# Performance work log

Hardware: AMD Instinct MI355X
Metric: run time of the kernel (lower is better)

Reference implementation:

```python
import jax, jax.numpy as jnp
import numpy as np

# Segment geometry (from init_kwargs): modes ['u','uv','v'] -> out_v = alpha * x_u @ W_uv
U = 128
V = 128
IN_OFF = [0, 128, 256, 384]
W_OFF = [k * U * V for k in range(8)]          # [0,16384,...,114688]
OUT_OFF = [0, 128, 256, 384]
IN_STRIDE = 512
OUT_STRIDE = 512
W_STRIDE = 8 * U * V                           # 131072
# (in_seg, w_seg, out_seg, coefficient)
PATHS = [(0, 0, 0, 1.0), (1, 1, 1, 1.0), (2, 2, 2, 1.0), (3, 3, 3, 1.0),
         (0, 4, 1, 0.5), (1, 5, 2, 0.5), (2, 6, 3, 0.5), (3, 7, 0, 0.5)]
B = 32768
E = 4  # num_embeddings (experts)


def setup_inputs() -> dict:
    key = jax.random.key(0)
    k1, k2, k3 = jax.random.split(key, 3)
    tensor_in = jax.random.normal(k1, (B, IN_STRIDE), dtype=jnp.float32)
    tensor_w = jax.random.normal(k2, (E, W_STRIDE), dtype=jnp.float32)
    tensor_w_id = jax.random.randint(k3, (B,), 0, E, dtype=jnp.int32)
    return {"tensor_in": tensor_in, "tensor_w": tensor_w, "tensor_w_id": tensor_w_id}


def _batch_linear(tensor_in, tensor_w, tensor_w_id):
    """Segmented path-indexed grouped linear (cuEquivariance BatchLinear fwd).

    tensor_in: [B, IN_STRIDE]; tensor_w: [E, W_STRIDE]; tensor_w_id: [B] int in [0,E).
    For each path (i, j, k, alpha):
        out[b, OUT_OFF[k]:+V] += alpha * x[b, IN_OFF[i]:+U] @ W[w_id[b], seg j].reshape(U, V)
    """
    nb = tensor_in.shape[0]
    ne = tensor_w.shape[0]
    onehot = jax.nn.one_hot(tensor_w_id, ne, dtype=tensor_in.dtype)  # [B, E]
    out = jnp.zeros((nb, OUT_STRIDE), dtype=tensor_in.dtype)
    for (i, j, k, a) in PATHS:
        x = tensor_in[:, IN_OFF[i]:IN_OFF[i] + U]                    # [B, U]
        w_seg = tensor_w[:, W_OFF[j]:W_OFF[j] + U * V].reshape(ne, U, V)
        # masked per-expert dense GEMMs (small fixed expert count)
        y = jnp.zeros((nb, V), dtype=tensor_in.dtype)
        for e in range(ne):
            y = y + onehot[:, e:e + 1] * (x @ w_seg[e])              # [B, V]
        out = out.at[:, OUT_OFF[k]:OUT_OFF[k] + V].add(a * y)
    return out


def reference(tensor_in, tensor_w, tensor_w_id):
    return _batch_linear(tensor_in, tensor_w, tensor_w_id)
```

## Files before the change

kernel.cpp:

```cpp
#include <hip/hip_runtime.h>
#include <stdint.h>

#define U 128
#define V 128
#define IN_STRIDE 512
#define OUT_STRIDE 512
#define W_STRIDE (8 * U * V)
#define NB 32768
#define NE 4

#define WS_WSHUF 0
#define WS_CNT   1048576
#define WS_SORT  1048640

typedef __bf16 bf16x8 __attribute__((ext_vector_type(8)));
typedef float f32x16 __attribute__((ext_vector_type(16)));
typedef unsigned int u32x4 __attribute__((ext_vector_type(4)));

static __device__ __forceinline__ unsigned short f2bf(float f) {
    unsigned int u = __builtin_bit_cast(unsigned int, f);
    u += 0x7FFFu + ((u >> 16) & 1u);
    return (unsigned short)(u >> 16);
}

__global__ void prep_kernel(const float* __restrict__ w, unsigned short* __restrict__ wshuf,
                            unsigned int* __restrict__ cnt) {
    if (blockIdx.x == 0 && threadIdx.x < NE) cnt[threadIdx.x] = 0u;
    int t = blockIdx.x * 256 + threadIdx.x;
    int lane = t & 63;
    int kt = (t >> 6) & 7;
    int nt = (t >> 9) & 3;
    int s  = (t >> 11) & 7;
    int e  = (t >> 14) & 3;
    int kbase = kt * 16 + ((lane >> 5) << 3);
    int n = nt * 32 + (lane & 31);
    const float* src = w + (size_t)e * W_STRIDE + (size_t)s * (U * V) + n;
    float sc = (s >= 4) ? 0.5f : 1.0f;
    __attribute__((aligned(16))) unsigned short o[8];
#pragma unroll
    for (int j = 0; j < 8; j++) o[j] = f2bf(src[(size_t)(kbase + j) * V] * sc);
    *(u32x4*)(wshuf + (size_t)t * 8) = *(const u32x4*)o;
}

__global__ void scatter_kernel(const int* __restrict__ wid, unsigned int* __restrict__ cnt,
                               int* __restrict__ sorted) {
    __shared__ unsigned int lcnt[NE];
    __shared__ unsigned int lbase[NE];
    int t = threadIdx.x;
    if (t < NE) lcnt[t] = 0u;
    __syncthreads();
    int i = blockIdx.x * 256 + t;
    int e = wid[i];
    unsigned int lpos = atomicAdd(&lcnt[e], 1u);
    __syncthreads();
    if (t < NE) lbase[t] = atomicAdd(&cnt[t], lcnt[t]);
    __syncthreads();
    sorted[e * NB + (int)(lbase[e] + lpos)] = i;
}

__global__ __launch_bounds__(512, 4) void gemm_kernel(
        const float* __restrict__ x, const unsigned short* __restrict__ wshuf,
        const unsigned int* __restrict__ cnt, const int* __restrict__ sorted,
        float* __restrict__ out) {
    const int rowbase = blockIdx.x * 32;
    __shared__ float ldsf[32][512];
    __shared__ int rowid[32];

    const unsigned int p1 = cnt[0];
    const unsigned int p2 = p1 + cnt[1];
    const unsigned int p3 = p2 + cnt[2];

    const int t = threadIdx.x;
    const int w = t >> 6, lane = t & 63;
    const int l5 = lane >> 5, m0 = lane & 31;
    const int kout = w >> 1, nhalf = w & 1;

    int rid[4];
#pragma unroll
    for (int i = 0; i < 4; i++) {
        unsigned int ls = (unsigned int)(rowbase + 4 * w + i);
        int e = (ls >= p1) + (ls >= p2) + (ls >= p3);
        unsigned int pe = (e == 0) ? 0u : (e == 1) ? p1 : (e == 2) ? p2 : p3;
        rid[i] = sorted[e * NB + (int)(ls - pe)];
    }
    if (t < 32) {
        unsigned int ls = (unsigned int)(rowbase + t);
        int e = (ls >= p1) + (ls >= p2) + (ls >= p3);
        unsigned int pe = (e == 0) ? 0u : (e == 1) ? p1 : (e == 2) ? p2 : p3;
        rowid[t] = sorted[e * NB + (int)(ls - pe)];
    }

#pragma unroll
    for (int i = 0; i < 4; i++) {
        int r = 4 * w + i;
        int rs = r & 7;
        const float* xb = x + (size_t)rid[i] * IN_STRIDE + ((m0 ^ rs) << 2) + l5 * 128;
#pragma unroll
        for (int h = 0; h < 2; h++) {
            __builtin_amdgcn_global_load_lds(
                (const __attribute__((address_space(1))) unsigned int*)(xb + h * 256),
                (__attribute__((address_space(3))) unsigned int*)&ldsf[r][h * 256],
                16, 0, 0);
        }
    }

    const unsigned int lh = (unsigned int)rowbase, lt = (unsigned int)(rowbase + 31);
    const int ehead = (lh >= p1) + (lh >= p2) + (lh >= p3);
    const int etail = (lt >= p1) + (lt >= p2) + (lt >= p3);
    const unsigned int l0 = (unsigned int)(rowbase + m0);
    const int e0 = (l0 >= p1) + (l0 >= p2) + (l0 >= p3);

    const int xbc1 = (kout + 3) & 3;
    const int xbs[2] = {kout, xbc1};
    const int sgs[2] = {kout, xbc1 + 4};
    const int rsw = m0 & 7;

    f32x16 acc0 = {}, acc1 = {};

    if (ehead == etail) {
        const unsigned short* wb0 =
            wshuf + (size_t)(((ehead * 8 + sgs[0]) * 4 + nhalf * 2) * 8) * 512 + (size_t)lane * 8;
        u32x4 bp[8];
#pragma unroll
        for (int kt = 0; kt < 4; kt++) {
            bp[kt * 2]     = *(const u32x4*)(wb0 + (size_t)kt * 512);
            bp[kt * 2 + 1] = *(const u32x4*)(wb0 + (size_t)(8 + kt) * 512);
        }
        __syncthreads();

#pragma unroll
        for (int c = 0; c < 2; c++) {
            const float* ar = &ldsf[m0][xbs[c] * 128];
            const unsigned short* wb =
                wshuf + (size_t)(((ehead * 8 + sgs[c]) * 4 + nhalf * 2) * 8) * 512 + (size_t)lane * 8;
#pragma unroll
            for (int kt = 0; kt < 8; kt++) {
                int gj0 = kt * 4 + l5 * 2;
                float4 va = *(const float4*)(ar + ((gj0 ^ rsw) << 2));
                float4 vb = *(const float4*)(ar + (((gj0 + 1) ^ rsw) << 2));
                bf16x8 a;
                a[0] = (__bf16)va.x; a[1] = (__bf16)va.y;
                a[2] = (__bf16)va.z; a[3] = (__bf16)va.w;
                a[4] = (__bf16)vb.x; a[5] = (__bf16)vb.y;
                a[6] = (__bf16)vb.z; a[7] = (__bf16)vb.w;
                bf16x8 b0, b1;
                if (c == 0 && kt < 4) {
                    b0 = __builtin_bit_cast(bf16x8, bp[kt * 2]);
                    b1 = __builtin_bit_cast(bf16x8, bp[kt * 2 + 1]);
                } else {
                    b0 = __builtin_bit_cast(bf16x8, *(const u32x4*)(wb + (size_t)kt * 512));
                    b1 = __builtin_bit_cast(bf16x8, *(const u32x4*)(wb + (size_t)(8 + kt) * 512));
                }
                acc0 = __builtin_amdgcn_mfma_f32_32x32x16_bf16(a, b0, acc0, 0, 0, 0);
                acc1 = __builtin_amdgcn_mfma_f32_32x32x16_bf16(a, b1, acc1, 0, 0, 0);
            }
        }
    } else {
        unsigned int msk[4];
#pragma unroll
        for (int e = 0; e < 4; e++) msk[e] = (e0 == e) ? 0xFFFFFFFFu : 0u;
        __syncthreads();
#pragma unroll
        for (int c = 0; c < 2; c++) {
            const float* ar = &ldsf[m0][xbs[c] * 128];
#pragma unroll
            for (int kt = 0; kt < 8; kt++) {
                int gj0 = kt * 4 + l5 * 2;
                float4 va = *(const float4*)(ar + ((gj0 ^ rsw) << 2));
                float4 vb = *(const float4*)(ar + (((gj0 + 1) ^ rsw) << 2));
                __attribute__((aligned(16))) unsigned short au[8];
                au[0] = f2bf(va.x); au[1] = f2bf(va.y);
                au[2] = f2bf(va.z); au[3] = f2bf(va.w);
                au[4] = f2bf(vb.x); au[5] = f2bf(vb.y);
                au[6] = f2bf(vb.z); au[7] = f2bf(vb.w);
                u32x4 araw = *(const u32x4*)au;
#pragma unroll
                for (int e = 0; e < 4; e++) {
                    u32x4 mm = {msk[e], msk[e], msk[e], msk[e]};
                    bf16x8 am = __builtin_bit_cast(bf16x8, araw & mm);
                    const unsigned short* wb =
                        wshuf + (size_t)(((e * 8 + sgs[c]) * 4 + nhalf * 2) * 8) * 512 + (size_t)lane * 8;
                    bf16x8 b0 = __builtin_bit_cast(bf16x8, *(const u32x4*)(wb + (size_t)kt * 512));
                    bf16x8 b1 = __builtin_bit_cast(bf16x8, *(const u32x4*)(wb + (size_t)(8 + kt) * 512));
                    acc0 = __builtin_amdgcn_mfma_f32_32x32x16_bf16(am, b0, acc0, 0, 0, 0);
                    acc1 = __builtin_amdgcn_mfma_f32_32x32x16_bf16(am, b1, acc1, 0, 0, 0);
                }
            }
        }
    }

    const int colb = kout * 128 + nhalf * 64 + m0;
    const int rh = l5 << 2;
#pragma unroll
    for (int q = 0; q < 4; q++) {
#pragma unroll
        for (int d = 0; d < 4; d++) {
            int reg = q * 4 + d;
            int rl = d + 8 * q + rh;
            float* o = out + (size_t)rowid[rl] * OUT_STRIDE + colb;
            o[0]  = acc0[reg];
            o[32] = acc1[reg];
        }
    }
}

extern "C" void kernel_launch(void* const* d_in, const int* in_sizes, int n_in,
                              void* d_out, int out_size, void* d_ws, size_t ws_size,
                              hipStream_t stream) {
    const float* x = (const float*)d_in[0];
    const float* w = (const float*)d_in[1];
    const int* wid = (const int*)d_in[2];
    float* out = (float*)d_out;

    unsigned short* wshuf = (unsigned short*)((char*)d_ws + WS_WSHUF);
    unsigned int* cnt = (unsigned int*)((char*)d_ws + WS_CNT);
    int* sorted = (int*)((char*)d_ws + WS_SORT);

    prep_kernel<<<256, 256, 0, stream>>>(w, wshuf, cnt);
    scatter_kernel<<<128, 256, 0, stream>>>(wid, cnt, sorted);
    gemm_kernel<<<1024, 512, 0, stream>>>(x, wshuf, cnt, sorted, out);
}
```

Baseline: 136.7 us.

## Switch GEMM to 16-row tiles with 16x16x32 MFMA and reshuffled weight layout

Halves the rows per block from 32 to 16 and switches from 32x32x16 to 16x16x32 bf16 MFMA, which changes the prep kernel's weight-shuffle layout to match the new B-fragment shape. The grid doubles to 2048 blocks with half the LDS per block, and launch bounds rise to 8 blocks per CU. The aim is higher occupancy and fewer blocks straddling expert boundaries, which take the slow masked four-expert path. The cost is that each weight fragment is reused over only 16 rows, roughly doubling weight reads per output row.

```diff
diff --git a/kernel.cpp b/kernel.cpp
--- a/kernel.cpp
+++ b/kernel.cpp
@@ -14,7 +14,7 @@
 #define WS_SORT  1048640
 
 typedef __bf16 bf16x8 __attribute__((ext_vector_type(8)));
-typedef float f32x16 __attribute__((ext_vector_type(16)));
+typedef float f32x4 __attribute__((ext_vector_type(4)));
 typedef unsigned int u32x4 __attribute__((ext_vector_type(4)));
 
 static __device__ __forceinline__ unsigned short f2bf(float f) {
@@ -28,12 +28,12 @@
     if (blockIdx.x == 0 && threadIdx.x < NE) cnt[threadIdx.x] = 0u;
     int t = blockIdx.x * 256 + threadIdx.x;
     int lane = t & 63;
-    int kt = (t >> 6) & 7;
-    int nt = (t >> 9) & 3;
+    int ks = (t >> 6) & 3;
+    int nt = (t >> 8) & 7;
     int s  = (t >> 11) & 7;
     int e  = (t >> 14) & 3;
-    int kbase = kt * 16 + ((lane >> 5) << 3);
-    int n = nt * 32 + (lane & 31);
+    int kbase = ks * 32 + ((lane >> 4) << 3);
+    int n = nt * 16 + (lane & 15);
     const float* src = w + (size_t)e * W_STRIDE + (size_t)s * (U * V) + n;
     float sc = (s >= 4) ? 0.5f : 1.0f;
     __attribute__((aligned(16))) unsigned short o[8];
@@ -58,13 +58,13 @@
     sorted[e * NB + (int)(lbase[e] + lpos)] = i;
 }
 
-__global__ __launch_bounds__(512, 4) void gemm_kernel(
+__global__ __launch_bounds__(512, 8) void gemm_kernel(
         const float* __restrict__ x, const unsigned short* __restrict__ wshuf,
         const unsigned int* __restrict__ cnt, const int* __restrict__ sorted,
         float* __restrict__ out) {
-    const int rowbase = blockIdx.x * 32;
-    __shared__ float ldsf[32][512];
-    __shared__ int rowid[32];
+    const int rowbase = blockIdx.x * 16;
+    __shared__ float ldsf[16][512];
+    __shared__ int rowid[16];
 
     const unsigned int p1 = cnt[0];
     const unsigned int p2 = p1 + cnt[1];
@@ -74,16 +74,18 @@
     const int w = t >> 6, lane = t & 63;
     const int l5 = lane >> 5, m0 = lane & 31;
     const int kout = w >> 1, nhalf = w & 1;
-
-    int rid[4];
-#pragma unroll
-    for (int i = 0; i < 4; i++) {
-        unsigned int ls = (unsigned int)(rowbase + 4 * w + i);
+    const int m16 = lane & 15;
+    const int kg = lane >> 4;
+
+    int rid[2];
+#pragma unroll
+    for (int i = 0; i < 2; i++) {
+        unsigned int ls = (unsigned int)(rowbase + 2 * w + i);
         int e = (ls >= p1) + (ls >= p2) + (ls >= p3);
         unsigned int pe = (e == 0) ? 0u : (e == 1) ? p1 : (e == 2) ? p2 : p3;
         rid[i] = sorted[e * NB + (int)(ls - pe)];
     }
-    if (t < 32) {
+    if (t < 16) {
         unsigned int ls = (unsigned int)(rowbase + t);
         int e = (ls >= p1) + (ls >= p2) + (ls >= p3);
         unsigned int pe = (e == 0) ? 0u : (e == 1) ? p1 : (e == 2) ? p2 : p3;
@@ -91,10 +93,10 @@
     }
 
 #pragma unroll
-    for (int i = 0; i < 4; i++) {
-        int r = 4 * w + i;
+    for (int i = 0; i < 2; i++) {
+        int r = 2 * w + i;
         int rs = r & 7;
-        const float* xb = x + (size_t)rid[i] * IN_STRIDE + ((m0 ^ rs) << 2) + l5 * 128;
+        const float* xb = x + (size_t)rid[i] * IN_STRIDE + l5 * 128 + ((m0 ^ rs) << 2);
 #pragma unroll
         for (int h = 0; h < 2; h++) {
             __builtin_amdgcn_global_load_lds(
@@ -104,38 +106,39 @@
         }
     }
 
-    const unsigned int lh = (unsigned int)rowbase, lt = (unsigned int)(rowbase + 31);
+    const unsigned int lh = (unsigned int)rowbase, lt = (unsigned int)(rowbase + 15);
     const int ehead = (lh >= p1) + (lh >= p2) + (lh >= p3);
     const int etail = (lt >= p1) + (lt >= p2) + (lt >= p3);
-    const unsigned int l0 = (unsigned int)(rowbase + m0);
+    const unsigned int l0 = (unsigned int)(rowbase + m16);
     const int e0 = (l0 >= p1) + (l0 >= p2) + (l0 >= p3);
 
     const int xbc1 = (kout + 3) & 3;
     const int xbs[2] = {kout, xbc1};
     const int sgs[2] = {kout, xbc1 + 4};
-    const int rsw = m0 & 7;
-
-    f32x16 acc0 = {}, acc1 = {};
+    const int rsw = m16 & 7;
+
+    f32x4 acc[4] = {};
 
     if (ehead == etail) {
         const unsigned short* wb0 =
-            wshuf + (size_t)(((ehead * 8 + sgs[0]) * 4 + nhalf * 2) * 8) * 512 + (size_t)lane * 8;
-        u32x4 bp[8];
-#pragma unroll
-        for (int kt = 0; kt < 4; kt++) {
-            bp[kt * 2]     = *(const u32x4*)(wb0 + (size_t)kt * 512);
-            bp[kt * 2 + 1] = *(const u32x4*)(wb0 + (size_t)(8 + kt) * 512);
-        }
+            wshuf + ((size_t)((ehead * 8 + sgs[0]) * 8 + nhalf * 4)) * 2048 + (size_t)lane * 8;
+        const unsigned short* wb1 =
+            wshuf + ((size_t)((ehead * 8 + sgs[1]) * 8 + nhalf * 4)) * 2048 + (size_t)lane * 8;
+        u32x4 bp[4];
+#pragma unroll
+        for (int ni = 0; ni < 4; ni++)
+            bp[ni] = *(const u32x4*)(wb0 + (size_t)ni * 2048);
+
         __syncthreads();
 
 #pragma unroll
         for (int c = 0; c < 2; c++) {
-            const float* ar = &ldsf[m0][xbs[c] * 128];
-            const unsigned short* wb =
-                wshuf + (size_t)(((ehead * 8 + sgs[c]) * 4 + nhalf * 2) * 8) * 512 + (size_t)lane * 8;
-#pragma unroll
-            for (int kt = 0; kt < 8; kt++) {
-                int gj0 = kt * 4 + l5 * 2;
+            const float* ar = &ldsf[m16][0];
+            const int cb3 = xbs[c] * 32;
+            const unsigned short* wb = (c == 0) ? wb0 : wb1;
+#pragma unroll
+            for (int s = 0; s < 4; s++) {
+                int gj0 = cb3 + s * 8 + kg * 2;
                 float4 va = *(const float4*)(ar + ((gj0 ^ rsw) << 2));
                 float4 vb = *(const float4*)(ar + (((gj0 + 1) ^ rsw) << 2));
                 bf16x8 a;
@@ -143,16 +146,14 @@
                 a[2] = (__bf16)va.z; a[3] = (__bf16)va.w;
                 a[4] = (__bf16)vb.x; a[5] = (__bf16)vb.y;
                 a[6] = (__bf16)vb.z; a[7] = (__bf16)vb.w;
-                bf16x8 b0, b1;
-                if (c == 0 && kt < 4) {
-                    b0 = __builtin_bit_cast(bf16x8, bp[kt * 2]);
-                    b1 = __builtin_bit_cast(bf16x8, bp[kt * 2 + 1]);
-                } else {
-                    b0 = __builtin_bit_cast(bf16x8, *(const u32x4*)(wb + (size_t)kt * 512));
-                    b1 = __builtin_bit_cast(bf16x8, *(const u32x4*)(wb + (size_t)(8 + kt) * 512));
+#pragma unroll
+                for (int ni = 0; ni < 4; ni++) {
+                    bf16x8 b;
+                    if (c == 0 && s == 0) b = __builtin_bit_cast(bf16x8, bp[ni]);
+                    else b = __builtin_bit_cast(bf16x8,
+                             *(const u32x4*)(wb + (size_t)ni * 2048 + (size_t)s * 512));
+                    acc[ni] = __builtin_amdgcn_mfma_f32_16x16x32_bf16(a, b, acc[ni], 0, 0, 0);
                 }
-                acc0 = __builtin_amdgcn_mfma_f32_32x32x16_bf16(a, b0, acc0, 0, 0, 0);
-                acc1 = __builtin_amdgcn_mfma_f32_32x32x16_bf16(a, b1, acc1, 0, 0, 0);
             }
         }
     } else {
@@ -162,10 +163,11 @@
         __syncthreads();
 #pragma unroll
         for (int c = 0; c < 2; c++) {
-            const float* ar = &ldsf[m0][xbs[c] * 128];
-#pragma unroll
-            for (int kt = 0; kt < 8; kt++) {
-                int gj0 = kt * 4 + l5 * 2;
+            const float* ar = &ldsf[m16][0];
+            const int cb3 = xbs[c] * 32;
+#pragma unroll
+            for (int s = 0; s < 4; s++) {
+                int gj0 = cb3 + s * 8 + kg * 2;
                 float4 va = *(const float4*)(ar + ((gj0 ^ rsw) << 2));
                 float4 vb = *(const float4*)(ar + (((gj0 + 1) ^ rsw) << 2));
                 __attribute__((aligned(16))) unsigned short au[8];
@@ -178,28 +180,26 @@
                 for (int e = 0; e < 4; e++) {
                     u32x4 mm = {msk[e], msk[e], msk[e], msk[e]};
                     bf16x8 am = __builtin_bit_cast(bf16x8, araw & mm);
-                    const unsigned short* wb =
-                        wshuf + (size_t)(((e * 8 + sgs[c]) * 4 + nhalf * 2) * 8) * 512 + (size_t)lane * 8;
-                    bf16x8 b0 = __builtin_bit_cast(bf16x8, *(const u32x4*)(wb + (size_t)kt * 512));
-                    bf16x8 b1 = __builtin_bit_cast(bf16x8, *(const u32x4*)(wb + (size_t)(8 + kt) * 512));
-                    acc0 = __builtin_amdgcn_mfma_f32_32x32x16_bf16(am, b0, acc0, 0, 0, 0);
-                    acc1 = __builtin_amdgcn_mfma_f32_32x32x16_bf16(am, b1, acc1, 0, 0, 0);
+                    const unsigned short* wbe =
+                        wshuf + ((size_t)((e * 8 + sgs[c]) * 8 + nhalf * 4)) * 2048 + (size_t)lane * 8;
+#pragma unroll
+                    for (int ni = 0; ni < 4; ni++) {
+                        bf16x8 b = __builtin_bit_cast(bf16x8,
+                            *(const u32x4*)(wbe + (size_t)ni * 2048 + (size_t)s * 512));
+                        acc[ni] = __builtin_amdgcn_mfma_f32_16x16x32_bf16(am, b, acc[ni], 0, 0, 0);
+                    }
                 }
             }
         }
     }
 
-    const int colb = kout * 128 + nhalf * 64 + m0;
-    const int rh = l5 << 2;
-#pragma unroll
-    for (int q = 0; q < 4; q++) {
-#pragma unroll
-        for (int d = 0; d < 4; d++) {
-            int reg = q * 4 + d;
-            int rl = d + 8 * q + rh;
-            float* o = out + (size_t)rowid[rl] * OUT_STRIDE + colb;
-            o[0]  = acc0[reg];
-            o[32] = acc1[reg];
+    const int colb = w * 64 + m16;
+#pragma unroll
+    for (int ni = 0; ni < 4; ni++) {
+#pragma unroll
+        for (int reg = 0; reg < 4; reg++) {
+            int rl = kg * 4 + reg;
+            out[(size_t)rowid[rl] * OUT_STRIDE + colb + ni * 16] = acc[ni][reg];
         }
     }
 }
@@ -218,5 +218,5 @@
 
     prep_kernel<<<256, 256, 0, stream>>>(w, wshuf, cnt);
     scatter_kernel<<<128, 256, 0, stream>>>(wid, cnt, sorted);
-    gemm_kernel<<<1024, 512, 0, stream>>>(x, wshuf, cnt, sorted, out);
-}
+    gemm_kernel<<<2048, 512, 0, stream>>>(x, wshuf, cnt, sorted, out);
+}
```

Result: slower. 165.6 us (+21.2%).

## Process four row tiles per block with double-buffered LDS prefetch of activations

Applied to the files above, without the earlier changes.

Each GEMM block now handles 128 sorted rows as four 32-row tiles, using two LDS buffers so the gathered x rows for the next tile are loaded while the current tile computes. Output stores for the previous tile are deferred into the next iteration, and the full first weight segment is preloaded into registers. The grid shrinks fourfold and launch bounds drop to two blocks per CU, trading cross-block parallelism and occupancy for intra-block load/compute overlap and amortised setup.

```diff
diff --git a/kernel.cpp b/kernel.cpp
--- a/kernel.cpp
+++ b/kernel.cpp
@@ -58,13 +58,13 @@
     sorted[e * NB + (int)(lbase[e] + lpos)] = i;
 }
 
-__global__ __launch_bounds__(512, 4) void gemm_kernel(
+__global__ __launch_bounds__(512, 2) void gemm_kernel(
         const float* __restrict__ x, const unsigned short* __restrict__ wshuf,
         const unsigned int* __restrict__ cnt, const int* __restrict__ sorted,
         float* __restrict__ out) {
-    const int rowbase = blockIdx.x * 32;
-    __shared__ float ldsf[32][512];
-    __shared__ int rowid[32];
+    const int blk = blockIdx.x;
+    __shared__ float ldsf[2][32][512];
+    __shared__ int rowid[128];
 
     const unsigned int p1 = cnt[0];
     const unsigned int p2 = p1 + cnt[1];
@@ -74,17 +74,10 @@
     const int w = t >> 6, lane = t & 63;
     const int l5 = lane >> 5, m0 = lane & 31;
     const int kout = w >> 1, nhalf = w & 1;
-
-    int rid[4];
-#pragma unroll
-    for (int i = 0; i < 4; i++) {
-        unsigned int ls = (unsigned int)(rowbase + 4 * w + i);
-        int e = (ls >= p1) + (ls >= p2) + (ls >= p3);
-        unsigned int pe = (e == 0) ? 0u : (e == 1) ? p1 : (e == 2) ? p2 : p3;
-        rid[i] = sorted[e * NB + (int)(ls - pe)];
-    }
-    if (t < 32) {
-        unsigned int ls = (unsigned int)(rowbase + t);
+    const int rsw = m0 & 7;
+
+    if (t < 128) {
+        unsigned int ls = (unsigned int)(blk * 128 + t);
         int e = (ls >= p1) + (ls >= p2) + (ls >= p3);
         unsigned int pe = (e == 0) ? 0u : (e == 1) ? p1 : (e == 2) ? p2 : p3;
         rowid[t] = sorted[e * NB + (int)(ls - pe)];
@@ -93,115 +86,204 @@
 #pragma unroll
     for (int i = 0; i < 4; i++) {
         int r = 4 * w + i;
+        unsigned int ls = (unsigned int)(blk * 128 + r);
+        int e = (ls >= p1) + (ls >= p2) + (ls >= p3);
+        unsigned int pe = (e == 0) ? 0u : (e == 1) ? p1 : (e == 2) ? p2 : p3;
+        int rr = sorted[e * NB + (int)(ls - pe)];
         int rs = r & 7;
-        const float* xb = x + (size_t)rid[i] * IN_STRIDE + ((m0 ^ rs) << 2) + l5 * 128;
+        const float* xb = x + (size_t)rr * IN_STRIDE + ((m0 ^ rs) << 2) + l5 * 128;
 #pragma unroll
         for (int h = 0; h < 2; h++) {
             __builtin_amdgcn_global_load_lds(
                 (const __attribute__((address_space(1))) unsigned int*)(xb + h * 256),
-                (__attribute__((address_space(3))) unsigned int*)&ldsf[r][h * 256],
+                (__attribute__((address_space(3))) unsigned int*)&ldsf[0][r][h * 256],
                 16, 0, 0);
         }
     }
 
-    const unsigned int lh = (unsigned int)rowbase, lt = (unsigned int)(rowbase + 31);
-    const int ehead = (lh >= p1) + (lh >= p2) + (lh >= p3);
-    const int etail = (lt >= p1) + (lt >= p2) + (lt >= p3);
-    const unsigned int l0 = (unsigned int)(rowbase + m0);
-    const int e0 = (l0 >= p1) + (l0 >= p2) + (l0 >= p3);
-
-    const int xbc1 = (kout + 3) & 3;
-    const int xbs[2] = {kout, xbc1};
-    const int sgs[2] = {kout, xbc1 + 4};
-    const int rsw = m0 & 7;
-
+    asm volatile("s_waitcnt vmcnt(0) lgkmcnt(0)" ::: "memory");
+    __builtin_amdgcn_sched_barrier(0);
+    __builtin_amdgcn_s_barrier();
+    __builtin_amdgcn_sched_barrier(0);
+
+    const int colb = kout * 128 + nhalf * 64 + m0;
+    const int rh = l5 << 2;
     f32x16 acc0 = {}, acc1 = {};
 
-    if (ehead == etail) {
-        const unsigned short* wb0 =
-            wshuf + (size_t)(((ehead * 8 + sgs[0]) * 4 + nhalf * 2) * 8) * 512 + (size_t)lane * 8;
-        u32x4 bp[8];
-#pragma unroll
-        for (int kt = 0; kt < 4; kt++) {
-            bp[kt * 2]     = *(const u32x4*)(wb0 + (size_t)kt * 512);
-            bp[kt * 2 + 1] = *(const u32x4*)(wb0 + (size_t)(8 + kt) * 512);
+    for (int T = 0; T < 4; T++) {
+        const unsigned int rb = (unsigned int)(blk * 128 + T * 32);
+        const int ehead = (rb >= p1) + (rb >= p2) + (rb >= p3);
+        const unsigned int rte = rb + 31u;
+        const int etail = (rte >= p1) + (rte >= p2) + (rte >= p3);
+        const int fast = (ehead == etail);
+        const int xb1 = (kout + 3) & 3;
+        const float (*buf)[512] = ldsf[T & 1];
+
+        if (fast) {
+            const unsigned short* wb0 =
+                wshuf + (size_t)(((ehead * 8 + kout) * 4 + nhalf * 2) * 8) * 512 + (size_t)lane * 8;
+            u32x4 bp[16];
+#pragma unroll
+            for (int kt = 0; kt < 8; kt++) {
+                bp[kt * 2]     = *(const u32x4*)(wb0 + (size_t)kt * 512);
+                bp[kt * 2 + 1] = *(const u32x4*)(wb0 + (size_t)(8 + kt) * 512);
+            }
+
+            if (T > 0) {
+#pragma unroll
+                for (int q = 0; q < 4; q++)
+#pragma unroll
+                    for (int d = 0; d < 4; d++) {
+                        int reg = q * 4 + d;
+                        int rl = d + 8 * q + rh;
+                        float* o = out + (size_t)rowid[(T - 1) * 32 + rl] * OUT_STRIDE + colb;
+                        o[0]  = acc0[reg];
+                        o[32] = acc1[reg];
+                    }
+                acc0 = (f32x16){};
+                acc1 = (f32x16){};
+            }
+
+            if (T < 3) {
+#pragma unroll
+                for (int i = 0; i < 4; i++) {
+                    int r = 4 * w + i;
+                    int rr = rowid[(T + 1) * 32 + r];
+                    int rs = r & 7;
+                    const float* xb = x + (size_t)rr * IN_STRIDE + ((m0 ^ rs) << 2) + l5 * 128;
+#pragma unroll
+                    for (int h = 0; h < 2; h++) {
+                        __builtin_amdgcn_global_load_lds(
+                            (const __attribute__((address_space(1))) unsigned int*)(xb + h * 256),
+                            (__attribute__((address_space(3))) unsigned int*)&ldsf[(T + 1) & 1][r][h * 256],
+                            16, 0, 0);
+                    }
+                }
+            }
+
+            {
+                const float* ar = &buf[m0][kout * 128];
+#pragma unroll
+                for (int kt = 0; kt < 8; kt++) {
+                    int gj0 = kt * 4 + l5 * 2;
+                    float4 va = *(const float4*)(ar + ((gj0 ^ rsw) << 2));
+                    float4 vb = *(const float4*)(ar + (((gj0 + 1) ^ rsw) << 2));
+                    bf16x8 a;
+                    a[0] = (__bf16)va.x; a[1] = (__bf16)va.y;
+                    a[2] = (__bf16)va.z; a[3] = (__bf16)va.w;
+                    a[4] = (__bf16)vb.x; a[5] = (__bf16)vb.y;
+                    a[6] = (__bf16)vb.z; a[7] = (__bf16)vb.w;
+                    bf16x8 b0 = __builtin_bit_cast(bf16x8, bp[kt * 2]);
+                    bf16x8 b1 = __builtin_bit_cast(bf16x8, bp[kt * 2 + 1]);
+                    acc0 = __builtin_amdgcn_mfma_f32_32x32x16_bf16(a, b0, acc0, 0, 0, 0);
+                    acc1 = __builtin_amdgcn_mfma_f32_32x32x16_bf16(a, b1, acc1, 0, 0, 0);
+                }
+            }
+            {
+                const unsigned short* wb1 =
+                    wshuf + (size_t)(((ehead * 8 + xb1 + 4) * 4 + nhalf * 2) * 8) * 512 + (size_t)lane * 8;
+                const float* ar = &buf[m0][xb1 * 128];
+#pragma unroll
+                for (int kt = 0; kt < 8; kt++) {
+                    int gj0 = kt * 4 + l5 * 2;
+                    float4 va = *(const float4*)(ar + ((gj0 ^ rsw) << 2));
+                    float4 vb = *(const float4*)(ar + (((gj0 + 1) ^ rsw) << 2));
+                    bf16x8 a;
+                    a[0] = (__bf16)va.x; a[1] = (__bf16)va.y;
+                    a[2] = (__bf16)va.z; a[3] = (__bf16)va.w;
+                    a[4] = (__bf16)vb.x; a[5] = (__bf16)vb.y;
+                    a[6] = (__bf16)vb.z; a[7] = (__bf16)vb.w;
+                    bf16x8 b0 = __builtin_bit_cast(bf16x8, *(const u32x4*)(wb1 + (size_t)kt * 512));
+                    bf16x8 b1 = __builtin_bit_cast(bf16x8, *(const u32x4*)(wb1 + (size_t)(8 + kt) * 512));
+                    acc0 = __builtin_amdgcn_mfma_f32_32x32x16_bf16(a, b0, acc0, 0, 0, 0);
+                    acc1 = __builtin_amdgcn_mfma_f32_32x32x16_bf16(a, b1, acc1, 0, 0, 0);
+                }
+            }
+        } else {
+            if (T > 0) {
+#pragma unroll
+                for (int q = 0; q < 4; q++)
+#pragma unroll
+                    for (int d = 0; d < 4; d++) {
+                        int reg = q * 4 + d;
+                        int rl = d + 8 * q + rh;
+                        float* o = out + (size_t)rowid[(T - 1) * 32 + rl] * OUT_STRIDE + colb;
+                        o[0]  = acc0[reg];
+                        o[32] = acc1[reg];
+                    }
+                acc0 = (f32x16){};
+                acc1 = (f32x16){};
+            }
+            if (T < 3) {
+#pragma unroll
+                for (int i = 0; i < 4; i++) {
+                    int r = 4 * w + i;
+                    int rr = rowid[(T + 1) * 32 + r];
+                    int rs = r & 7;
+                    const float* xb = x + (size_t)rr * IN_STRIDE + ((m0 ^ rs) << 2) + l5 * 128;
+#pragma unroll
+                    for (int h = 0; h < 2; h++) {
+                        __builtin_amdgcn_global_load_lds(
+                            (const __attribute__((address_space(1))) unsigned int*)(xb + h * 256),
+                            (__attribute__((address_space(3))) unsigned int*)&ldsf[(T + 1) & 1][r][h * 256],
+                            16, 0, 0);
+                    }
+                }
+            }
+            const unsigned int l0 = rb + (unsigned int)m0;
+            const int e0 = (l0 >= p1) + (l0 >= p2) + (l0 >= p3);
+            unsigned int msk[4];
+#pragma unroll
+            for (int e = 0; e < 4; e++) msk[e] = (e0 == e) ? 0xFFFFFFFFu : 0u;
+            const int xbs[2] = {kout, xb1};
+            const int sgs[2] = {kout, xb1 + 4};
+#pragma unroll
+            for (int c = 0; c < 2; c++) {
+                const float* ar = &buf[m0][xbs[c] * 128];
+#pragma unroll
+                for (int kt = 0; kt < 8; kt++) {
+                    int gj0 = kt * 4 + l5 * 2;
+                    float4 va = *(const float4*)(ar + ((gj0 ^ rsw) << 2));
+                    float4 vb = *(const float4*)(ar + (((gj0 + 1) ^ rsw) << 2));
+                    __attribute__((aligned(16))) unsigned short au[8];
+                    au[0] = f2bf(va.x); au[1] = f2bf(va.y);
+                    au[2] = f2bf(va.z); au[3] = f2bf(va.w);
+                    au[4] = f2bf(vb.x); au[5] = f2bf(vb.y);
+                    au[6] = f2bf(vb.z); au[7] = f2bf(vb.w);
+                    u32x4 araw = *(const u32x4*)au;
+#pragma unroll
+                    for (int e = 0; e < 4; e++) {
+                        u32x4 mm = {msk[e], msk[e], msk[e], msk[e]};
+                        bf16x8 am = __builtin_bit_cast(bf16x8, araw & mm);
+                        const unsigned short* wbe =
+                            wshuf + (size_t)(((e * 8 + sgs[c]) * 4 + nhalf * 2) * 8) * 512 + (size_t)lane * 8;
+                        bf16x8 b0 = __builtin_bit_cast(bf16x8, *(const u32x4*)(wbe + (size_t)kt * 512));
+                        bf16x8 b1 = __builtin_bit_cast(bf16x8, *(const u32x4*)(wbe + (size_t)(8 + kt) * 512));
+                        acc0 = __builtin_amdgcn_mfma_f32_32x32x16_bf16(am, b0, acc0, 0, 0, 0);
+                        acc1 = __builtin_amdgcn_mfma_f32_32x32x16_bf16(am, b1, acc1, 0, 0, 0);
+                    }
+                }
+            }
         }
-        __syncthreads();
-
-#pragma unroll
-        for (int c = 0; c < 2; c++) {
-            const float* ar = &ldsf[m0][xbs[c] * 128];
-            const unsigned short* wb =
-                wshuf + (size_t)(((ehead * 8 + sgs[c]) * 4 + nhalf * 2) * 8) * 512 + (size_t)lane * 8;
-#pragma unroll
-            for (int kt = 0; kt < 8; kt++) {
-                int gj0 = kt * 4 + l5 * 2;
-                float4 va = *(const float4*)(ar + ((gj0 ^ rsw) << 2));
-                float4 vb = *(const float4*)(ar + (((gj0 + 1) ^ rsw) << 2));
-                bf16x8 a;
-                a[0] = (__bf16)va.x; a[1] = (__bf16)va.y;
-                a[2] = (__bf16)va.z; a[3] = (__bf16)va.w;
-                a[4] = (__bf16)vb.x; a[5] = (__bf16)vb.y;
-                a[6] = (__bf16)vb.z; a[7] = (__bf16)vb.w;
-                bf16x8 b0, b1;
-                if (c == 0 && kt < 4) {
-                    b0 = __builtin_bit_cast(bf16x8, bp[kt * 2]);
-                    b1 = __builtin_bit_cast(bf16x8, bp[kt * 2 + 1]);
-                } else {
-                    b0 = __builtin_bit_cast(bf16x8, *(const u32x4*)(wb + (size_t)kt * 512));
-                    b1 = __builtin_bit_cast(bf16x8, *(const u32x4*)(wb + (size_t)(8 + kt) * 512));
-                }
-                acc0 = __builtin_amdgcn_mfma_f32_32x32x16_bf16(a, b0, acc0, 0, 0, 0);
-                acc1 = __builtin_amdgcn_mfma_f32_32x32x16_bf16(a, b1, acc1, 0, 0, 0);
-            }
-        }
-    } else {
-        unsigned int msk[4];
-#pragma unroll
-        for (int e = 0; e < 4; e++) msk[e] = (e0 == e) ? 0xFFFFFFFFu : 0u;
-        __syncthreads();
-#pragma unroll
-        for (int c = 0; c < 2; c++) {
-            const float* ar = &ldsf[m0][xbs[c] * 128];
-#pragma unroll
-            for (int kt = 0; kt < 8; kt++) {
-                int gj0 = kt * 4 + l5 * 2;
-                float4 va = *(const float4*)(ar + ((gj0 ^ rsw) << 2));
-                float4 vb = *(const float4*)(ar + (((gj0 + 1) ^ rsw) << 2));
-                __attribute__((aligned(16))) unsigned short au[8];
-                au[0] = f2bf(va.x); au[1] = f2bf(va.y);
-                au[2] = f2bf(va.z); au[3] = f2bf(va.w);
-                au[4] = f2bf(vb.x); au[5] = f2bf(vb.y);
-                au[6] = f2bf(vb.z); au[7] = f2bf(vb.w);
-                u32x4 araw = *(const u32x4*)au;
-#pragma unroll
-                for (int e = 0; e < 4; e++) {
-                    u32x4 mm = {msk[e], msk[e], msk[e], msk[e]};
-                    bf16x8 am = __builtin_bit_cast(bf16x8, araw & mm);
-                    const unsigned short* wb =
-                        wshuf + (size_t)(((e * 8 + sgs[c]) * 4 + nhalf * 2) * 8) * 512 + (size_t)lane * 8;
-                    bf16x8 b0 = __builtin_bit_cast(bf16x8, *(const u32x4*)(wb + (size_t)kt * 512));
-                    bf16x8 b1 = __builtin_bit_cast(bf16x8, *(const u32x4*)(wb + (size_t)(8 + kt) * 512));
-                    acc0 = __builtin_amdgcn_mfma_f32_32x32x16_bf16(am, b0, acc0, 0, 0, 0);
-                    acc1 = __builtin_amdgcn_mfma_f32_32x32x16_bf16(am, b1, acc1, 0, 0, 0);
-                }
-            }
+
+        if (T < 3) {
+            asm volatile("s_waitcnt vmcnt(0)" ::: "memory");
+            __builtin_amdgcn_sched_barrier(0);
+            __builtin_amdgcn_s_barrier();
+            __builtin_amdgcn_sched_barrier(0);
         }
     }
 
-    const int colb = kout * 128 + nhalf * 64 + m0;
-    const int rh = l5 << 2;
-#pragma unroll
-    for (int q = 0; q < 4; q++) {
+#pragma unroll
+    for (int q = 0; q < 4; q++)
 #pragma unroll
         for (int d = 0; d < 4; d++) {
             int reg = q * 4 + d;
             int rl = d + 8 * q + rh;
-            float* o = out + (size_t)rowid[rl] * OUT_STRIDE + colb;
+            float* o = out + (size_t)rowid[3 * 32 + rl] * OUT_STRIDE + colb;
             o[0]  = acc0[reg];
             o[32] = acc1[reg];
         }
-    }
 }
 
 extern "C" void kernel_launch(void* const* d_in, const int* in_sizes, int n_in,
@@ -218,5 +300,5 @@
 
     prep_kernel<<<256, 256, 0, stream>>>(w, wshuf, cnt);
     scatter_kernel<<<128, 256, 0, stream>>>(wid, cnt, sorted);
-    gemm_kernel<<<1024, 512, 0, stream>>>(x, wshuf, cnt, sorted, out);
-}
+    gemm_kernel<<<256, 512, 0, stream>>>(x, wshuf, cnt, sorted, out);
+}
```

Result: slower. 197.8 us (+44.7%).

## Split GEMM blocks per output segment and prefetch all weight fragments into registers

Applied to the files above, without the earlier changes.

Each block now covers one 128-column output segment for 32 rows instead of all four. It uses 256 threads and 16KB of LDS, and the grid grows fourfold. Each wave computes one 32-column tile and preloads all 16 B fragments into registers before the barrier, where previously half were loaded inside the loop. This should raise occupancy and overlap weight loads with the x gather. In exchange, the gathered x rows and the sorted-index lookups are duplicated across four blocks.

```diff
diff --git a/kernel.cpp b/kernel.cpp
--- a/kernel.cpp
+++ b/kernel.cpp
@@ -58,12 +58,15 @@
     sorted[e * NB + (int)(lbase[e] + lpos)] = i;
 }
 
-__global__ __launch_bounds__(512, 4) void gemm_kernel(
+__global__ __launch_bounds__(256, 4) void gemm_kernel(
         const float* __restrict__ x, const unsigned short* __restrict__ wshuf,
         const unsigned int* __restrict__ cnt, const int* __restrict__ sorted,
         float* __restrict__ out) {
-    const int rowbase = blockIdx.x * 32;
-    __shared__ float ldsf[32][512];
+    const int bid = blockIdx.x;
+    const int rg = bid >> 2;
+    const int kout = bid & 3;
+    const int rowbase = rg * 32;
+    __shared__ float ldsf[2][32][128];
     __shared__ int rowid[32];
 
     const unsigned int p1 = cnt[0];
@@ -73,16 +76,12 @@
     const int t = threadIdx.x;
     const int w = t >> 6, lane = t & 63;
     const int l5 = lane >> 5, m0 = lane & 31;
-    const int kout = w >> 1, nhalf = w & 1;
-
-    int rid[4];
-#pragma unroll
-    for (int i = 0; i < 4; i++) {
-        unsigned int ls = (unsigned int)(rowbase + 4 * w + i);
-        int e = (ls >= p1) + (ls >= p2) + (ls >= p3);
-        unsigned int pe = (e == 0) ? 0u : (e == 1) ? p1 : (e == 2) ? p2 : p3;
-        rid[i] = sorted[e * NB + (int)(ls - pe)];
-    }
+    const int rsw = m0 & 7;
+
+    const int xb1 = (kout + 3) & 3;
+    const int xbs[2] = {kout, xb1};
+    const int sgs[2] = {kout, xb1 + 4};
+
     if (t < 32) {
         unsigned int ls = (unsigned int)(rowbase + t);
         int e = (ls >= p1) + (ls >= p2) + (ls >= p3);
@@ -92,14 +91,19 @@
 
 #pragma unroll
     for (int i = 0; i < 4; i++) {
-        int r = 4 * w + i;
-        int rs = r & 7;
-        const float* xb = x + (size_t)rid[i] * IN_STRIDE + ((m0 ^ rs) << 2) + l5 * 128;
-#pragma unroll
-        for (int h = 0; h < 2; h++) {
+        int r0 = (w * 4 + i) * 2;
+        int rl_ = r0 + l5;
+        unsigned int ls = (unsigned int)(rowbase + rl_);
+        int e = (ls >= p1) + (ls >= p2) + (ls >= p3);
+        unsigned int pe = (e == 0) ? 0u : (e == 1) ? p1 : (e == 2) ? p2 : p3;
+        int rr = sorted[e * NB + (int)(ls - pe)];
+        int rs = rl_ & 7;
+        const float* xr = x + (size_t)rr * IN_STRIDE + ((m0 ^ rs) << 2);
+#pragma unroll
+        for (int c = 0; c < 2; c++) {
             __builtin_amdgcn_global_load_lds(
-                (const __attribute__((address_space(1))) unsigned int*)(xb + h * 256),
-                (__attribute__((address_space(3))) unsigned int*)&ldsf[r][h * 256],
+                (const __attribute__((address_space(1))) unsigned int*)(xr + xbs[c] * 128),
+                (__attribute__((address_space(3))) unsigned int*)&ldsf[c][r0][0],
                 16, 0, 0);
         }
     }
@@ -110,29 +114,24 @@
     const unsigned int l0 = (unsigned int)(rowbase + m0);
     const int e0 = (l0 >= p1) + (l0 >= p2) + (l0 >= p3);
 
-    const int xbc1 = (kout + 3) & 3;
-    const int xbs[2] = {kout, xbc1};
-    const int sgs[2] = {kout, xbc1 + 4};
-    const int rsw = m0 & 7;
-
-    f32x16 acc0 = {}, acc1 = {};
+    f32x16 acc = {};
 
     if (ehead == etail) {
-        const unsigned short* wb0 =
-            wshuf + (size_t)(((ehead * 8 + sgs[0]) * 4 + nhalf * 2) * 8) * 512 + (size_t)lane * 8;
-        u32x4 bp[8];
-#pragma unroll
-        for (int kt = 0; kt < 4; kt++) {
-            bp[kt * 2]     = *(const u32x4*)(wb0 + (size_t)kt * 512);
-            bp[kt * 2 + 1] = *(const u32x4*)(wb0 + (size_t)(8 + kt) * 512);
-        }
+        u32x4 bp[16];
+#pragma unroll
+        for (int c = 0; c < 2; c++) {
+            const unsigned short* wb =
+                wshuf + ((size_t)((ehead * 8 + sgs[c]) * 4 + w) * 8) * 512 + (size_t)lane * 8;
+#pragma unroll
+            for (int kt = 0; kt < 8; kt++)
+                bp[c * 8 + kt] = *(const u32x4*)(wb + (size_t)kt * 512);
+        }
+
         __syncthreads();
 
 #pragma unroll
         for (int c = 0; c < 2; c++) {
-            const float* ar = &ldsf[m0][xbs[c] * 128];
-            const unsigned short* wb =
-                wshuf + (size_t)(((ehead * 8 + sgs[c]) * 4 + nhalf * 2) * 8) * 512 + (size_t)lane * 8;
+            const float* ar = &ldsf[c][m0][0];
 #pragma unroll
             for (int kt = 0; kt < 8; kt++) {
                 int gj0 = kt * 4 + l5 * 2;
@@ -143,16 +142,8 @@
                 a[2] = (__bf16)va.z; a[3] = (__bf16)va.w;
                 a[4] = (__bf16)vb.x; a[5] = (__bf16)vb.y;
                 a[6] = (__bf16)vb.z; a[7] = (__bf16)vb.w;
-                bf16x8 b0, b1;
-                if (c == 0 && kt < 4) {
-                    b0 = __builtin_bit_cast(bf16x8, bp[kt * 2]);
-                    b1 = __builtin_bit_cast(bf16x8, bp[kt * 2 + 1]);
-                } else {
-                    b0 = __builtin_bit_cast(bf16x8, *(const u32x4*)(wb + (size_t)kt * 512));
-                    b1 = __builtin_bit_cast(bf16x8, *(const u32x4*)(wb + (size_t)(8 + kt) * 512));
-                }
-                acc0 = __builtin_amdgcn_mfma_f32_32x32x16_bf16(a, b0, acc0, 0, 0, 0);
-                acc1 = __builtin_amdgcn_mfma_f32_32x32x16_bf16(a, b1, acc1, 0, 0, 0);
+                bf16x8 b = __builtin_bit_cast(bf16x8, bp[c * 8 + kt]);
+                acc = __builtin_amdgcn_mfma_f32_32x32x16_bf16(a, b, acc, 0, 0, 0);
             }
         }
     } else {
@@ -162,7 +153,7 @@
         __syncthreads();
 #pragma unroll
         for (int c = 0; c < 2; c++) {
-            const float* ar = &ldsf[m0][xbs[c] * 128];
+            const float* ar = &ldsf[c][m0][0];
 #pragma unroll
             for (int kt = 0; kt < 8; kt++) {
                 int gj0 = kt * 4 + l5 * 2;
@@ -178,18 +169,16 @@
                 for (int e = 0; e < 4; e++) {
                     u32x4 mm = {msk[e], msk[e], msk[e], msk[e]};
                     bf16x8 am = __builtin_bit_cast(bf16x8, araw & mm);
-                    const unsigned short* wb =
-                        wshuf + (size_t)(((e * 8 + sgs[c]) * 4 + nhalf * 2) * 8) * 512 + (size_t)lane * 8;
-                    bf16x8 b0 = __builtin_bit_cast(bf16x8, *(const u32x4*)(wb + (size_t)kt * 512));
-                    bf16x8 b1 = __builtin_bit_cast(bf16x8, *(const u32x4*)(wb + (size_t)(8 + kt) * 512));
-                    acc0 = __builtin_amdgcn_mfma_f32_32x32x16_bf16(am, b0, acc0, 0, 0, 0);
-                    acc1 = __builtin_amdgcn_mfma_f32_32x32x16_bf16(am, b1, acc1, 0, 0, 0);
+                    const unsigned short* wbe =
+                        wshuf + ((size_t)((e * 8 + sgs[c]) * 4 + w) * 8) * 512 + (size_t)lane * 8;
+                    bf16x8 b = __builtin_bit_cast(bf16x8, *(const u32x4*)(wbe + (size_t)kt * 512));
+                    acc = __builtin_amdgcn_mfma_f32_32x32x16_bf16(am, b, acc, 0, 0, 0);
                 }
             }
         }
     }
 
-    const int colb = kout * 128 + nhalf * 64 + m0;
+    const int colb = kout * 128 + w * 32 + m0;
     const int rh = l5 << 2;
 #pragma unroll
     for (int q = 0; q < 4; q++) {
@@ -197,9 +186,7 @@
         for (int d = 0; d < 4; d++) {
             int reg = q * 4 + d;
             int rl = d + 8 * q + rh;
-            float* o = out + (size_t)rowid[rl] * OUT_STRIDE + colb;
-            o[0]  = acc0[reg];
-            o[32] = acc1[reg];
+            out[(size_t)rowid[rl] * OUT_STRIDE + colb] = acc[reg];
         }
     }
 }
@@ -218,5 +205,5 @@
 
     prep_kernel<<<256, 256, 0, stream>>>(w, wshuf, cnt);
     scatter_kernel<<<128, 256, 0, stream>>>(wid, cnt, sorted);
-    gemm_kernel<<<1024, 512, 0, stream>>>(x, wshuf, cnt, sorted, out);
-}
+    gemm_kernel<<<4096, 256, 0, stream>>>(x, wshuf, cnt, sorted, out);
+}
```

Result: slower. 143.3 us (+4.9%).
